# Kernel tuning notes

Measured on AMD Instinct MI355X. Metric: run time of the kernel, lower is better.

The kernel has to match this reference:

```python
import jax, jax.numpy as jnp
import numpy as np

T, D, HID = 32768, 256, 32


def setup_inputs() -> dict:
    key = jax.random.key(0)
    ks = jax.random.split(key, 16)
    # observation times in [84, 168], dose times in [0, 84] (so every t has a prior dose)
    t_abs = 84.0 + 84.0 * jax.random.uniform(ks[0], (T,), dtype=jnp.float32)
    dose_times_abs = jnp.sort(84.0 * jax.random.uniform(ks[1], (D,), dtype=jnp.float32))
    amts = 100.0 * jax.random.uniform(ks[2], (D,), dtype=jnp.float32)
    ss = (jax.random.uniform(ks[3], (D,), dtype=jnp.float32) > 0.5).astype(jnp.float32)
    ii = 24.0 * jax.random.uniform(ks[4], (D,), dtype=jnp.float32)
    span_phys = jnp.float32(168.0)
    # MLP params (torch Linear layout transposed: x @ W + b), scaled ~1/sqrt(fan_in)
    def lin(k, fi, fo):
        kw, kb = jax.random.split(k)
        s = 1.0 / np.sqrt(fi)
        return (jax.random.uniform(kw, (fi, fo), jnp.float32, -s, s),
                jax.random.uniform(kb, (fo,), jnp.float32, -s, s))
    W1, b1 = lin(ks[5], 5, HID)
    W2, b2 = lin(ks[6], HID, HID)
    W3, b3 = lin(ks[7], HID, HID)
    W4, b4 = lin(ks[8], HID, 1)
    log_sigma_phys = jnp.log(jnp.float32(10.0))
    return dict(t_abs=t_abs, dose_times_abs=dose_times_abs, amts=amts, ss=ss, ii=ii,
                span_phys=span_phys, log_sigma_phys=log_sigma_phys,
                W1=W1, b1=b1, W2=W2, b2=b2, W3=W3, b3=b3, W4=W4, b4=b4)


def reference(t_abs, dose_times_abs, amts, ss, ii, span_phys, log_sigma_phys,
              W1, b1, W2, b2, W3, b3, W4, b4):
    # pairwise normalized time-since-dose grid [T, D]
    dt = (t_abs[:, None] - dose_times_abs[None, :]) / span_phys
    mask = (dt >= 0.0).astype(dt.dtype)
    dt_masked = jnp.where(dt >= 0.0, dt, jnp.inf)
    dt_last = jnp.min(dt_masked, axis=-1, keepdims=True)  # [T, 1], time since last dose
    eps = 1e-6
    ss_norm = ss / (span_phys + eps)
    ii_norm = ii / (span_phys + eps)
    shp = dt.shape
    feats = jnp.stack([
        dt,
        jnp.broadcast_to(jnp.log1p(amts)[None, :], shp),
        jnp.broadcast_to(dt_last, shp),
        jnp.broadcast_to(ss_norm[None, :], shp),
        jnp.broadcast_to(ii_norm[None, :], shp),
    ], axis=-1)  # [T, D, 5]
    h = jax.nn.silu(feats @ W1 + b1)
    h = jax.nn.silu(h @ W2 + b2)
    h = jax.nn.silu(h @ W3 + b3)
    scores = (h @ W4 + b4)[..., 0]  # [T, D]
    sigma = jnp.exp(log_sigma_phys).astype(dt.dtype)
    w = mask * jnp.exp(-0.5 * (dt / sigma) ** 2)
    return (scores * w).sum(axis=-1)  # [T]
```

## Files before the change

kernel.cpp:

```cpp
#include <hip/hip_runtime.h>
#include <hip/hip_bf16.h>
#include <math.h>

#define T_N 32768
#define D_N 256
#define HID 32
#define LOG2E 1.44269504f
#define LN2   0.69314718f

typedef short  s16x8  __attribute__((ext_vector_type(8)));
typedef float  f32x16 __attribute__((ext_vector_type(16)));
typedef float  f32x4  __attribute__((ext_vector_type(4)));
typedef float  f32x2  __attribute__((ext_vector_type(2)));

union FragU { s16x8 v; unsigned u[4]; unsigned short s[8]; };

static __device__ __forceinline__ unsigned short w2b(float f) {
    union { __hip_bfloat16 h; unsigned short s; } u;
    u.h = __float2bfloat16(f); return u.s;
}
static __device__ __forceinline__ unsigned pkrh(float a, float b) {
    const unsigned ua = __float_as_uint(a) + 0x8000u;
    const unsigned ub = __float_as_uint(b) + 0x8000u;
#if __has_builtin(__builtin_amdgcn_perm)
    return __builtin_amdgcn_perm(ub, ua, 0x07060302u);
#else
    return (ua >> 16) | (ub & 0xFFFF0000u);
#endif
}
static __device__ __forceinline__ void pl32(unsigned &a, unsigned &b) {
    asm("v_permlane32_swap_b32 %0, %1" : "+v"(a), "+v"(b));
}
static __device__ __forceinline__ float exp2neg(float t) {
#if __has_builtin(__builtin_amdgcn_exp2f)
    return __builtin_amdgcn_exp2f(-t);
#else
    return __expf(-t * LN2);
#endif
}
static __device__ __forceinline__ void act4(float t0, float t1, float t2, float t3,
                                            f32x2 &o01, f32x2 &o23) {
    f32x2 e01; e01[0] = exp2neg(t0); e01[1] = exp2neg(t1);
    f32x2 e23; e23[0] = exp2neg(t2); e23[1] = exp2neg(t3);
    const f32x2 d01 = e01 + 1.0f;
    const f32x2 d23 = e23 + 1.0f;
    const f32x2 pp  = d01 * d23;
    const float r   = __builtin_amdgcn_rcpf(pp[0] * pp[1]);
    f32x2 rs; rs[0] = r * pp[1]; rs[1] = r * pp[0];
    const f32x2 i01 = rs * d23;
    const f32x2 i23 = rs * d01;
    f32x2 T01; T01[0] = t0; T01[1] = t1;
    f32x2 T23; T23[0] = t2; T23[1] = t3;
    o01 = T01 * i01;
    o23 = T23 * i23;
}
static __device__ __forceinline__ unsigned pk2(f32x2 v) { return pkrh(v[0], v[1]); }

__global__ __launch_bounds__(256, 3) void dose_encoder_kernel(
    const float* __restrict__ t_abs,
    const float* __restrict__ dose_t,
    const float* __restrict__ amts,
    const float* __restrict__ ss,
    const float* __restrict__ ii,
    const float* __restrict__ span_p,
    const float* __restrict__ logsig_p,
    const float* __restrict__ W1, const float* __restrict__ b1,
    const float* __restrict__ W2, const float* __restrict__ b2,
    const float* __restrict__ W3, const float* __restrict__ b3,
    const float* __restrict__ W4, const float* __restrict__ b4,
    float* __restrict__ out)
{
    __shared__ f32x4 pd[D_N];

    const int tid  = threadIdx.x;
    const int wv   = tid >> 6;
    const int lane = tid & 63;
    const int n    = lane & 31;
    const int hh   = lane >> 5;
    const int t    = blockIdx.x * 4 + wv;

    const float span   = span_p[0];
    const float inv_se = 1.0f / (span + 1e-6f);
    const float inv_sp = 1.0f / span;
    const float sigma  = __expf(logsig_p[0]);
    const float gk     = sqrtf(0.5f * LOG2E) / sigma;

    { f32x4 e;
      e[0] = dose_t[tid];
      e[1] = __uint_as_float(((unsigned)w2b(log1pf(amts[tid]))) |
                             ((unsigned)w2b(ss[tid] * inv_se) << 16));
      e[2] = __uint_as_float((unsigned)w2b(ii[tid] * inv_se));
      e[3] = 0.0f;
      pd[tid] = e; }
    __syncthreads();

    const float tv  = t_abs[t];
    const float dtl = (tv - dose_t[D_N - 1]) * inv_sp;

    FragU a1;
    {
        const int kmap[5] = {0, 2, 1, 3, 4};
        #pragma unroll
        for (int j = 0; j < 8; ++j) {
            const int k = hh * 8 + j;
            a1.s[j] = (k < 5) ? w2b(LOG2E * W1[kmap[k] * HID + n]) : (unsigned short)0;
        }
    }
    FragU a2[2], a3[2];
    #pragma unroll
    for (int mf = 0; mf < 2; ++mf)
        #pragma unroll
        for (int j = 0; j < 8; ++j) {
            const int k = mf * 16 + hh * 8 + j;
            a2[mf].s[j] = w2b(W2[k * HID + n]);
            a3[mf].s[j] = w2b(W3[k * HID + n]);
        }
    f32x16 c1, c2, c3; f32x2 w4p[8];
    #pragma unroll
    for (int r = 0; r < 16; ++r) {
        const int row = (r & 3) + 8 * (r >> 2) + 4 * hh;
        c1[r] = LOG2E * b1[row];
        c2[r] = LOG2E * b2[row];
        c3[r] = LOG2E * b3[row];
        w4p[r >> 1][r & 1] = LN2 * W4[row];
    }
    const float b4s = b4[0];

    float acc = 0.0f;
    #pragma unroll 2
    for (int c = 0; c < 8; ++c) {
        const f32x4 p   = pd[c * 32 + n];
        const float dtv = (tv - p[0]) * inv_sp;

        FragU bf;
        bf.u[0] = pkrh(dtv, dtl);
        bf.u[1] = __float_as_uint(p[1]);
        bf.u[2] = __float_as_uint(p[2]);
        bf.u[3] = 0u;

        f32x16 h = __builtin_amdgcn_mfma_f32_32x32x16_bf16(a1.v, bf.v, c1, 0, 0, 0);

        FragU bh0, bh1;
        {
            f32x2 s0, s1, s2, s3, s4, s5, s6, s7;
            act4(h[0],  h[1],  h[2],  h[3],  s0, s1);
            act4(h[4],  h[5],  h[6],  h[7],  s2, s3);
            act4(h[8],  h[9],  h[10], h[11], s4, s5);
            act4(h[12], h[13], h[14], h[15], s6, s7);
            unsigned wx0 = pk2(s0), wy0 = pk2(s1);
            unsigned wx1 = pk2(s2), wy1 = pk2(s3);
            unsigned wx2 = pk2(s4), wy2 = pk2(s5);
            unsigned wx3 = pk2(s6), wy3 = pk2(s7);
            pl32(wx0, wx1); pl32(wy0, wy1); pl32(wx2, wx3); pl32(wy2, wy3);
            bh0.u[0] = wx0; bh0.u[1] = wy0; bh0.u[2] = wx1; bh0.u[3] = wy1;
            bh1.u[0] = wx2; bh1.u[1] = wy2; bh1.u[2] = wx3; bh1.u[3] = wy3;
        }

        h = __builtin_amdgcn_mfma_f32_32x32x16_bf16(a2[0].v, bh0.v, c2, 0, 0, 0);
        h = __builtin_amdgcn_mfma_f32_32x32x16_bf16(a2[1].v, bh1.v, h,  0, 0, 0);

        {
            f32x2 s0, s1, s2, s3, s4, s5, s6, s7;
            act4(h[0],  h[1],  h[2],  h[3],  s0, s1);
            act4(h[4],  h[5],  h[6],  h[7],  s2, s3);
            act4(h[8],  h[9],  h[10], h[11], s4, s5);
            act4(h[12], h[13], h[14], h[15], s6, s7);
            unsigned wx0 = pk2(s0), wy0 = pk2(s1);
            unsigned wx1 = pk2(s2), wy1 = pk2(s3);
            unsigned wx2 = pk2(s4), wy2 = pk2(s5);
            unsigned wx3 = pk2(s6), wy3 = pk2(s7);
            pl32(wx0, wx1); pl32(wy0, wy1); pl32(wx2, wx3); pl32(wy2, wy3);
            bh0.u[0] = wx0; bh0.u[1] = wy0; bh0.u[2] = wx1; bh0.u[3] = wy1;
            bh1.u[0] = wx2; bh1.u[1] = wy2; bh1.u[2] = wx3; bh1.u[3] = wy3;
        }

        h = __builtin_amdgcn_mfma_f32_32x32x16_bf16(a3[0].v, bh0.v, c3, 0, 0, 0);
        h = __builtin_amdgcn_mfma_f32_32x32x16_bf16(a3[1].v, bh1.v, h,  0, 0, 0);

        f32x2 pacc = {0.0f, 0.0f};
        #pragma unroll
        for (int g = 0; g < 4; ++g) {
            f32x2 oa, ob;
            act4(h[4*g], h[4*g+1], h[4*g+2], h[4*g+3], oa, ob);
            pacc += oa * w4p[2*g];
            pacc += ob * w4p[2*g + 1];
        }
        float part = pacc[0] + pacc[1];
        part += __shfl_xor(part, 32, 64);
        const float score = part + b4s;

        const float q   = dtv * gk;
        float wgt = exp2neg(q * q);
        wgt = (dtv >= 0.0f) ? wgt : 0.0f;
        acc = fmaf(score, wgt, acc);
    }

    #pragma unroll
    for (int off = 1; off < 32; off <<= 1)
        acc += __shfl_xor(acc, off, 64);
    if (lane == 0) out[t] = acc;
}

extern "C" void kernel_launch(void* const* d_in, const int* in_sizes, int n_in,
                              void* d_out, int out_size, void* d_ws, size_t ws_size,
                              hipStream_t stream) {
    const float* t_abs  = (const float*)d_in[0];
    const float* dose_t = (const float*)d_in[1];
    const float* amts   = (const float*)d_in[2];
    const float* ss     = (const float*)d_in[3];
    const float* ii     = (const float*)d_in[4];
    const float* span_p = (const float*)d_in[5];
    const float* logsig = (const float*)d_in[6];
    const float* W1 = (const float*)d_in[7];
    const float* b1 = (const float*)d_in[8];
    const float* W2 = (const float*)d_in[9];
    const float* b2 = (const float*)d_in[10];
    const float* W3 = (const float*)d_in[11];
    const float* b3 = (const float*)d_in[12];
    const float* W4 = (const float*)d_in[13];
    const float* b4 = (const float*)d_in[14];
    float* out = (float*)d_out;

    dose_encoder_kernel<<<dim3(T_N / 4), dim3(256), 0, stream>>>(
        t_abs, dose_t, amts, ss, ii, span_p, logsig,
        W1, b1, W2, b2, W3, b3, W4, b4, out);
}
```

Baseline: 246.4 us.

## Process two query times per wave to interleave independent MFMA chains

Each wave now handles two observation times at once, running two independent MLP chains (A and B) that share the same dose features and weight fragments. Interleaving them lets each chain's MFMA latency overlap with the other's activation math, and halves the grid so per-block setup (weight loads, shared-memory dose table) is amortized over twice as many outputs. In exchange, register pressure roughly doubles for accumulators, which risks spills or lower occupancy under the 3-blocks-per-CU bound, and the loop unroll drops from 2 to 1.

```diff
diff --git a/kernel.cpp b/kernel.cpp
--- a/kernel.cpp
+++ b/kernel.cpp
@@ -56,6 +56,32 @@
 }
 static __device__ __forceinline__ unsigned pk2(f32x2 v) { return pkrh(v[0], v[1]); }
 
+static __device__ __forceinline__ void actsec(const f32x16 &h, FragU &bh0, FragU &bh1) {
+    f32x2 s0, s1, s2, s3, s4, s5, s6, s7;
+    act4(h[0],  h[1],  h[2],  h[3],  s0, s1);
+    act4(h[4],  h[5],  h[6],  h[7],  s2, s3);
+    act4(h[8],  h[9],  h[10], h[11], s4, s5);
+    act4(h[12], h[13], h[14], h[15], s6, s7);
+    unsigned wx0 = pk2(s0), wy0 = pk2(s1);
+    unsigned wx1 = pk2(s2), wy1 = pk2(s3);
+    unsigned wx2 = pk2(s4), wy2 = pk2(s5);
+    unsigned wx3 = pk2(s6), wy3 = pk2(s7);
+    pl32(wx0, wx1); pl32(wy0, wy1); pl32(wx2, wx3); pl32(wy2, wy3);
+    bh0.u[0] = wx0; bh0.u[1] = wy0; bh0.u[2] = wx1; bh0.u[3] = wy1;
+    bh1.u[0] = wx2; bh1.u[1] = wy2; bh1.u[2] = wx3; bh1.u[3] = wy3;
+}
+static __device__ __forceinline__ float headsec(const f32x16 &h, const f32x2 *w4p) {
+    f32x2 pacc = {0.0f, 0.0f};
+    #pragma unroll
+    for (int g = 0; g < 4; ++g) {
+        f32x2 oa, ob;
+        act4(h[4*g], h[4*g+1], h[4*g+2], h[4*g+3], oa, ob);
+        pacc += oa * w4p[2*g];
+        pacc += ob * w4p[2*g + 1];
+    }
+    return pacc[0] + pacc[1];
+}
+
 __global__ __launch_bounds__(256, 3) void dose_encoder_kernel(
     const float* __restrict__ t_abs,
     const float* __restrict__ dose_t,
@@ -77,7 +103,7 @@
     const int lane = tid & 63;
     const int n    = lane & 31;
     const int hh   = lane >> 5;
-    const int t    = blockIdx.x * 4 + wv;
+    const int t0   = blockIdx.x * 8 + wv * 2;
 
     const float span   = span_p[0];
     const float inv_se = 1.0f / (span + 1e-6f);
@@ -94,8 +120,11 @@
       pd[tid] = e; }
     __syncthreads();
 
-    const float tv  = t_abs[t];
-    const float dtl = (tv - dose_t[D_N - 1]) * inv_sp;
+    const float tvA = t_abs[t0];
+    const float tvB = t_abs[t0 + 1];
+    const float lastd = dose_t[D_N - 1];
+    const float dtlA = (tvA - lastd) * inv_sp;
+    const float dtlB = (tvB - lastd) * inv_sp;
 
     FragU a1;
     {
@@ -126,79 +155,63 @@
     }
     const float b4s = b4[0];
 
-    float acc = 0.0f;
-    #pragma unroll 2
+    float accA = 0.0f, accB = 0.0f;
+    #pragma unroll 1
     for (int c = 0; c < 8; ++c) {
-        const f32x4 p   = pd[c * 32 + n];
-        const float dtv = (tv - p[0]) * inv_sp;
-
-        FragU bf;
-        bf.u[0] = pkrh(dtv, dtl);
-        bf.u[1] = __float_as_uint(p[1]);
-        bf.u[2] = __float_as_uint(p[2]);
-        bf.u[3] = 0u;
-
-        f32x16 h = __builtin_amdgcn_mfma_f32_32x32x16_bf16(a1.v, bf.v, c1, 0, 0, 0);
-
-        FragU bh0, bh1;
-        {
-            f32x2 s0, s1, s2, s3, s4, s5, s6, s7;
-            act4(h[0],  h[1],  h[2],  h[3],  s0, s1);
-            act4(h[4],  h[5],  h[6],  h[7],  s2, s3);
-            act4(h[8],  h[9],  h[10], h[11], s4, s5);
-            act4(h[12], h[13], h[14], h[15], s6, s7);
-            unsigned wx0 = pk2(s0), wy0 = pk2(s1);
-            unsigned wx1 = pk2(s2), wy1 = pk2(s3);
-            unsigned wx2 = pk2(s4), wy2 = pk2(s5);
-            unsigned wx3 = pk2(s6), wy3 = pk2(s7);
-            pl32(wx0, wx1); pl32(wy0, wy1); pl32(wx2, wx3); pl32(wy2, wy3);
-            bh0.u[0] = wx0; bh0.u[1] = wy0; bh0.u[2] = wx1; bh0.u[3] = wy1;
-            bh1.u[0] = wx2; bh1.u[1] = wy2; bh1.u[2] = wx3; bh1.u[3] = wy3;
-        }
-
-        h = __builtin_amdgcn_mfma_f32_32x32x16_bf16(a2[0].v, bh0.v, c2, 0, 0, 0);
-        h = __builtin_amdgcn_mfma_f32_32x32x16_bf16(a2[1].v, bh1.v, h,  0, 0, 0);
-
-        {
-            f32x2 s0, s1, s2, s3, s4, s5, s6, s7;
-            act4(h[0],  h[1],  h[2],  h[3],  s0, s1);
-            act4(h[4],  h[5],  h[6],  h[7],  s2, s3);
-            act4(h[8],  h[9],  h[10], h[11], s4, s5);
-            act4(h[12], h[13], h[14], h[15], s6, s7);
-            unsigned wx0 = pk2(s0), wy0 = pk2(s1);
-            unsigned wx1 = pk2(s2), wy1 = pk2(s3);
-            unsigned wx2 = pk2(s4), wy2 = pk2(s5);
-            unsigned wx3 = pk2(s6), wy3 = pk2(s7);
-            pl32(wx0, wx1); pl32(wy0, wy1); pl32(wx2, wx3); pl32(wy2, wy3);
-            bh0.u[0] = wx0; bh0.u[1] = wy0; bh0.u[2] = wx1; bh0.u[3] = wy1;
-            bh1.u[0] = wx2; bh1.u[1] = wy2; bh1.u[2] = wx3; bh1.u[3] = wy3;
-        }
-
-        h = __builtin_amdgcn_mfma_f32_32x32x16_bf16(a3[0].v, bh0.v, c3, 0, 0, 0);
-        h = __builtin_amdgcn_mfma_f32_32x32x16_bf16(a3[1].v, bh1.v, h,  0, 0, 0);
-
-        f32x2 pacc = {0.0f, 0.0f};
-        #pragma unroll
-        for (int g = 0; g < 4; ++g) {
-            f32x2 oa, ob;
-            act4(h[4*g], h[4*g+1], h[4*g+2], h[4*g+3], oa, ob);
-            pacc += oa * w4p[2*g];
-            pacc += ob * w4p[2*g + 1];
-        }
-        float part = pacc[0] + pacc[1];
-        part += __shfl_xor(part, 32, 64);
-        const float score = part + b4s;
-
-        const float q   = dtv * gk;
-        float wgt = exp2neg(q * q);
-        wgt = (dtv >= 0.0f) ? wgt : 0.0f;
-        acc = fmaf(score, wgt, acc);
-    }
-
-    #pragma unroll
-    for (int off = 1; off < 32; off <<= 1)
-        acc += __shfl_xor(acc, off, 64);
-    if (lane == 0) out[t] = acc;
+        const f32x4 p    = pd[c * 32 + n];
+        const float dtvA = (tvA - p[0]) * inv_sp;
+        const float dtvB = (tvB - p[0]) * inv_sp;
+
+        FragU bfA, bfB;
+        bfA.u[0] = pkrh(dtvA, dtlA);
+        bfB.u[0] = pkrh(dtvB, dtlB);
+        bfA.u[1] = bfB.u[1] = __float_as_uint(p[1]);
+        bfA.u[2] = bfB.u[2] = __float_as_uint(p[2]);
+        bfA.u[3] = bfB.u[3] = 0u;
+
+        f32x16 hA = __builtin_amdgcn_mfma_f32_32x32x16_bf16(a1.v, bfA.v, c1, 0, 0, 0);
+        f32x16 hB = __builtin_amdgcn_mfma_f32_32x32x16_bf16(a1.v, bfB.v, c1, 0, 0, 0);
+
+        FragU bhA0, bhA1, bhB0, bhB1;
+        actsec(hA, bhA0, bhA1);
+        actsec(hB, bhB0, bhB1);
+
+        hA = __builtin_amdgcn_mfma_f32_32x32x16_bf16(a2[0].v, bhA0.v, c2, 0, 0, 0);
+        hA = __builtin_amdgcn_mfma_f32_32x32x16_bf16(a2[1].v, bhA1.v, hA, 0, 0, 0);
+        hB = __builtin_amdgcn_mfma_f32_32x32x16_bf16(a2[0].v, bhB0.v, c2, 0, 0, 0);
+        hB = __builtin_amdgcn_mfma_f32_32x32x16_bf16(a2[1].v, bhB1.v, hB, 0, 0, 0);
+
+        actsec(hA, bhA0, bhA1);
+        actsec(hB, bhB0, bhB1);
+
+        hA = __builtin_amdgcn_mfma_f32_32x32x16_bf16(a3[0].v, bhA0.v, c3, 0, 0, 0);
+        hA = __builtin_amdgcn_mfma_f32_32x32x16_bf16(a3[1].v, bhA1.v, hA, 0, 0, 0);
+        hB = __builtin_amdgcn_mfma_f32_32x32x16_bf16(a3[0].v, bhB0.v, c3, 0, 0, 0);
+        hB = __builtin_amdgcn_mfma_f32_32x32x16_bf16(a3[1].v, bhB1.v, hB, 0, 0, 0);
+
+        float partA = headsec(hA, w4p);
+        float partB = headsec(hB, w4p);
+        partA += __shfl_xor(partA, 32, 64);
+        partB += __shfl_xor(partB, 32, 64);
+        const float scoreA = partA + b4s;
+        const float scoreB = partB + b4s;
+
+        const float qA = dtvA * gk;
+        const float qB = dtvB * gk;
+        float wgtA = exp2neg(qA * qA);
+        float wgtB = exp2neg(qB * qB);
+        wgtA = (dtvA >= 0.0f) ? wgtA : 0.0f;
+        wgtB = (dtvB >= 0.0f) ? wgtB : 0.0f;
+        accA = fmaf(scoreA, wgtA, accA);
+        accB = fmaf(scoreB, wgtB, accB);
+    }
+
+    #pragma unroll
+    for (int off = 1; off < 32; off <<= 1) {
+        accA += __shfl_xor(accA, off, 64);
+        accB += __shfl_xor(accB, off, 64);
+    }
+    if (lane == 0) { out[t0] = accA; out[t0 + 1] = accB; }
 }
 
 extern "C" void kernel_launch(void* const* d_in, const int* in_sizes, int n_in,
@@ -221,7 +234,7 @@
     const float* b4 = (const float*)d_in[14];
     float* out = (float*)d_out;
 
-    dose_encoder_kernel<<<dim3(T_N / 4), dim3(256), 0, stream>>>(
+    dose_encoder_kernel<<<dim3(T_N / 8), dim3(256), 0, stream>>>(
         t_abs, dose_t, amts, ss, ii, span_p, logsig,
         W1, b1, W2, b2, W3, b3, W4, b4, out);
 }
```

Result: faster. 234.5 us (-4.8%).
